# Kernel tuning notes

Hardware: AMD Instinct MI355X
Metric: run time of the kernel (lower is better)

The kernel has to match this reference:

```python
import jax, jax.numpy as jnp
import numpy as np

B, L, H = 4, 2048, 1024
NQ, NKV, D = 8, 2, 256
I, V = 3584, 16384
EPS = 1e-6
THETA = 1e7
ROPE_DIM = 64

def rmsnorm(x, w, eps=EPS):
    xf = x.astype(jnp.float32)
    rms = jax.lax.rsqrt(jnp.mean(xf * xf, axis=-1, keepdims=True) + eps)
    return (xf * rms).astype(x.dtype) * w

def apply_rope(x, positions):
    # x: [B, H, L, D]; rotate first ROPE_DIM dims, interleaved pairs
    n_pairs = ROPE_DIM // 2
    inv_freq = THETA ** (-2.0 * jnp.arange(n_pairs, dtype=jnp.float32) / ROPE_DIM)
    freqs = positions.astype(jnp.float32)[:, None] * inv_freq[None, :]  # [L, n_pairs]
    cos = jnp.cos(freqs)[None, None, :, :]
    sin = jnp.sin(freqs)[None, None, :, :]
    b, h, l, d = x.shape
    xr = x[..., :ROPE_DIM].reshape(b, h, l, n_pairs, 2)
    x0, x1 = xr[..., 0], xr[..., 1]
    r0 = x0 * cos - x1 * sin
    r1 = x0 * sin + x1 * cos
    rotated = jnp.stack([r0, r1], axis=-1).reshape(b, h, l, ROPE_DIM)
    return jnp.concatenate([rotated, x[..., ROPE_DIM:]], axis=-1)

def setup_inputs() -> dict:
    key = jax.random.key(0)
    ks = jax.random.split(key, 12)
    s = 0.02
    return {
        "embeddings": jax.random.normal(ks[0], (B, L, H), jnp.float32),
        "hidden_states": jax.random.normal(ks[1], (B, L, H), jnp.float32),
        "pre_emb_w": jnp.ones((H,), jnp.float32),
        "pre_hid_w": jnp.ones((H,), jnp.float32),
        "fc_w": jax.random.normal(ks[2], (H, 2 * H), jnp.float32) * s,
        "in_ln_w": jnp.ones((H,), jnp.float32),
        "q_w": jax.random.normal(ks[3], (2 * NQ * D, H), jnp.float32) * s,
        "k_w": jax.random.normal(ks[4], (NKV * D, H), jnp.float32) * s,
        "v_w": jax.random.normal(ks[5], (NKV * D, H), jnp.float32) * s,
        "o_w": jax.random.normal(ks[6], (H, NQ * D), jnp.float32) * s,
        "qn_w": jnp.ones((D,), jnp.float32),
        "kn_w": jnp.ones((D,), jnp.float32),
        "post_ln_w": jnp.ones((H,), jnp.float32),
        "gate_w": jax.random.normal(ks[7], (I, H), jnp.float32) * s,
        "up_w": jax.random.normal(ks[8], (I, H), jnp.float32) * s,
        "down_w": jax.random.normal(ks[9], (H, I), jnp.float32) * s,
        "norm_w": jnp.ones((H,), jnp.float32),
        "lm_w": jax.random.normal(ks[10], (V, H), jnp.float32) * s,
    }

def _attention(x, q_w, k_w, v_w, o_w, qn_w, kn_w):
    b, l, _ = x.shape
    qg = (x @ q_w.T).reshape(b, l, NQ, 2, D)
    q = qg[:, :, :, 0, :]
    gate = qg[:, :, :, 1, :]
    k = (x @ k_w.T).reshape(b, l, NKV, D)
    v = (x @ v_w.T).reshape(b, l, NKV, D)
    q = rmsnorm(q, qn_w)
    k = rmsnorm(k, kn_w)
    groups = NQ // NKV
    k = jnp.repeat(k, groups, axis=2)  # [B, L, NQ, D]
    v = jnp.repeat(v, groups, axis=2)
    q, k, v = (t.transpose(0, 2, 1, 3) for t in (q, k, v))  # [B, NQ, L, D]
    positions = jnp.arange(l)
    q = apply_rope(q, positions)
    k = apply_rope(k, positions)
    scores = jnp.einsum('bhqd,bhkd->bhqk', q, k) / jnp.sqrt(jnp.float32(D))
    causal = jnp.tril(jnp.ones((l, l), jnp.bool_))
    scores = jnp.where(causal[None, None], scores, jnp.finfo(scores.dtype).min)
    attn = jax.nn.softmax(scores, axis=-1)
    out = jnp.einsum('bhqk,bhkd->bhqd', attn, v)
    out = out.transpose(0, 2, 1, 3).reshape(b, l, NQ * D)
    out = out * jax.nn.sigmoid(gate.reshape(b, l, NQ * D))
    return out @ o_w.T

def reference(embeddings, hidden_states, pre_emb_w, pre_hid_w, fc_w, in_ln_w,
              q_w, k_w, v_w, o_w, qn_w, kn_w, post_ln_w, gate_w, up_w, down_w,
              norm_w, lm_w):
    x = jnp.concatenate([rmsnorm(embeddings, pre_emb_w),
                         rmsnorm(hidden_states, pre_hid_w)], axis=-1)
    x = x @ fc_w.T
    residual = x
    x = rmsnorm(x, in_ln_w)
    x = _attention(x, q_w, k_w, v_w, o_w, qn_w, kn_w)
    x = residual + x
    residual = x
    x = rmsnorm(x, post_ln_w)
    x = (jax.nn.silu(x @ gate_w.T) * (x @ up_w.T)) @ down_w.T
    x = residual + x
    x = rmsnorm(x, norm_w)
    return x @ lm_w.T
```

## Files before the change

kernel.cpp:

```cpp
#include <hip/hip_runtime.h>

typedef __bf16 bf16;
typedef __bf16 bf16x8 __attribute__((ext_vector_type(8)));
typedef __bf16 bf16x4 __attribute__((ext_vector_type(4)));
typedef float f32x4 __attribute__((ext_vector_type(4)));

__device__ inline f32x4 mfma16(bf16x8 a, bf16x8 b, f32x4 c) {
    return __builtin_amdgcn_mfma_f32_16x16x32_bf16(a, b, c, 0, 0, 0);
}

__device__ __forceinline__ void async_cp16(const void* g, void* l) {
    __builtin_amdgcn_global_load_lds(
        (__attribute__((address_space(1))) char*)g,
        (__attribute__((address_space(3))) char*)l,
        16, 0, 0);
}

__global__ __launch_bounds__(256) void w2b_kernel(const float* __restrict__ s,
                                                  bf16* __restrict__ d)
{
    const size_t i = ((size_t)blockIdx.x * 256 + threadIdx.x) * 4;
    const float4 f = *(const float4*)(s + i);
    bf16x4 t;
    t[0] = (bf16)f.x; t[1] = (bf16)f.y; t[2] = (bf16)f.z; t[3] = (bf16)f.w;
    *(bf16x4*)(d + i) = t;
}

__global__ __launch_bounds__(256) void w2b_qkv_kernel(
    const float* __restrict__ qw, const float* __restrict__ kw,
    const float* __restrict__ vw, bf16* __restrict__ dq)
{
    int bid = blockIdx.x;
    const float* s; bf16* d;
    if (bid < 4096)      { s = qw; d = dq; }
    else if (bid < 4608) { s = kw; d = dq + 4194304; bid -= 4096; }
    else                 { s = vw; d = dq + 4718592; bid -= 4608; }
    const size_t i = ((size_t)bid * 256 + threadIdx.x) * 4;
    const float4 f = *(const float4*)(s + i);
    bf16x4 t;
    t[0] = (bf16)f.x; t[1] = (bf16)f.y; t[2] = (bf16)f.z; t[3] = (bf16)f.w;
    *(bf16x4*)(d + i) = t;
}

__global__ __launch_bounds__(256) void w2b_gu_kernel(
    const float* __restrict__ gw, const float* __restrict__ uw, bf16* __restrict__ dg)
{
    int bid = blockIdx.x;
    const float* s; bf16* d;
    if (bid < 3584) { s = gw; d = dg; }
    else            { s = uw; d = dg + 3670016; bid -= 3584; }
    const size_t i = ((size_t)bid * 256 + threadIdx.x) * 4;
    const float4 f = *(const float4*)(s + i);
    bf16x4 t;
    t[0] = (bf16)f.x; t[1] = (bf16)f.y; t[2] = (bf16)f.z; t[3] = (bf16)f.w;
    *(bf16x4*)(d + i) = t;
}

template <int EPI>
__global__ __launch_bounds__(256) void gemm_kernel(
    const bf16* __restrict__ A, const bf16* __restrict__ B,
    const float* __restrict__ res, float* __restrict__ Cout,
    int M, int N, int K)
{
    __shared__ bf16 As[2][128][64];
    __shared__ bf16 Bs[2][128][64];
    const int tid = threadIdx.x;
    const int wave = tid >> 6, lane = tid & 63;
    const int quad = lane >> 4, l16 = lane & 15;
    const int xsw = l16 & 7;

    const int nby = M >> 7, nbx = N >> 7;
    const int nwg = nbx * nby;
    int bid = blockIdx.x;
    {
        const int q = nwg >> 3, r = nwg & 7;
        const int x = bid & 7, loc = bid >> 3;
        bid = (x < r ? x * (q + 1) : r * (q + 1) + (x - r) * q) + loc;
    }
    const int pg = nbx << 3;
    const int g = bid / pg, rem = bid - g * pg;
    const int by = (g << 3) + (rem & 7);
    const int bx = rem >> 3;
    const int row0 = by << 7, col0 = bx << 7;
    const int wrow = ((wave >> 1) << 6), wcol = ((wave & 1) << 6);

    f32x4 acc[4][4] = {};

    const int srow = tid >> 3;
    const int scol = ((tid & 7) ^ (srow & 7)) * 8;
    const bf16* Ag = A + (size_t)(row0 + srow) * K + scol;
    const bf16* Bg = B + (size_t)(col0 + srow) * K + scol;
    const size_t K32 = (size_t)32 * K;

#define STG128(BUF, KB) do { \
    _Pragma("unroll") for (int q = 0; q < 4; ++q) { \
        async_cp16(Ag + q * K32 + (KB), &As[BUF][0][0] + q * 2048 + wave * 512); \
        async_cp16(Bg + q * K32 + (KB), &Bs[BUF][0][0] + q * 2048 + wave * 512); } } while (0)

    const int NT = K >> 6;
    STG128(0, 0);
    __syncthreads();
    for (int t = 0; t < NT; ++t) {
        const int c = t & 1, n = c ^ 1;
        if (t + 1 < NT) STG128(n, (t + 1) * 64);
        bf16x8 af[8], bfr[8];
#pragma unroll
        for (int i = 0; i < 4; ++i) {
            af[i * 2 + 0] = *(const bf16x8*)(&As[c][wrow + i * 16 + l16][(quad ^ xsw) * 8]);
            af[i * 2 + 1] = *(const bf16x8*)(&As[c][wrow + i * 16 + l16][((4 + quad) ^ xsw) * 8]);
        }
#pragma unroll
        for (int j = 0; j < 4; ++j) {
            bfr[j * 2 + 0] = *(const bf16x8*)(&Bs[c][wcol + j * 16 + l16][(quad ^ xsw) * 8]);
            bfr[j * 2 + 1] = *(const bf16x8*)(&Bs[c][wcol + j * 16 + l16][((4 + quad) ^ xsw) * 8]);
        }
#pragma unroll
        for (int i = 0; i < 4; ++i)
#pragma unroll
            for (int j = 0; j < 4; ++j) {
                acc[i][j] = mfma16(af[i * 2 + 0], bfr[j * 2 + 0], acc[i][j]);
                acc[i][j] = mfma16(af[i * 2 + 1], bfr[j * 2 + 1], acc[i][j]);
            }
        __syncthreads();
    }
#undef STG128

#pragma unroll
    for (int i = 0; i < 4; ++i) {
        const int row = row0 + wrow + i * 16 + quad * 4;
#pragma unroll
        for (int j = 0; j < 4; ++j) {
            const int col = col0 + wcol + j * 16 + l16;
#pragma unroll
            for (int r = 0; r < 4; ++r) {
                const size_t idx = (size_t)(row + r) * N + col;
                float v = acc[i][j][r];
                if (EPI == 1) Cout[idx] = v + res[idx];
                else          Cout[idx] = v;
            }
        }
    }
}

template <int EPI>
__global__ __launch_bounds__(512, 2) void gemm256_kernel(
    const bf16* __restrict__ A, const bf16* __restrict__ B,
    const float* __restrict__ res, float* __restrict__ Cout,
    bf16* __restrict__ hout, int M, int N, int K)
{
    __shared__ bf16 As[2][2][128][64];
    __shared__ bf16 Bs[2][2][128][64];
    const int tid = threadIdx.x;
    const int wid = tid >> 6, lane = tid & 63;
    const int quad = lane >> 4, l16 = lane & 15;
    const int wm = wid >> 2, wn = wid & 3;
    const int xsw = l16 & 7;
    const int bofs = (wn & 1) * 64;

    const int nby = M >> 8, nbx = N >> 8;
    const int nwg = nbx * nby;
    int bid = blockIdx.x;
    {
        const int q = nwg >> 3, r = nwg & 7;
        const int x = bid & 7, loc = bid >> 3;
        bid = (x < r ? x * (q + 1) : r * (q + 1) + (x - r) * q) + loc;
    }
    const int pg = nbx << 3;
    const int g = bid / pg, rem = bid - g * pg;
    const int by = (g << 3) + (rem & 7);
    const int bx = rem >> 3;
    const int row0 = by << 8, col0 = bx << 8;

    const int srow = tid >> 3;
    const int scol = ((tid & 7) ^ ((tid >> 3) & 7)) * 8;
    const bf16* Abase = A + (size_t)(row0 + srow) * K + scol;
    const bf16* Bbase = B + (size_t)(col0 + srow) * K + scol;
    const size_t K64 = (size_t)K * 64;
    const size_t K128 = (size_t)K * 128;

    f32x4 acc[8][4] = {};
    bf16x8 af[8], bf0[4], bf1[4];

#define STG_A(BUF, HH, KB) do { \
    const bf16* _g = Abase + (size_t)(HH) * K128 + (KB); \
    bf16* _l = &As[BUF][HH][0][0] + wid * 512; \
    async_cp16(_g, _l); \
    async_cp16(_g + K64, _l + 4096); } while (0)
#define STG_B(BUF, HH, KB) do { \
    const bf16* _g = Bbase + (size_t)(HH) * K128 + (KB); \
    bf16* _l = &Bs[BUF][HH][0][0] + wid * 512; \
    async_cp16(_g, _l); \
    async_cp16(_g + K64, _l + 4096); } while (0)

#define RD_A(BUF, RH) do { \
    const bf16 (*Ah_)[64] = As[BUF][wm]; \
    _Pragma("unroll") for (int f = 0; f < 4; ++f) { \
        af[f*2+0] = *(const bf16x8*)(&Ah_[(RH)*64 + f*16 + l16][(quad ^ xsw) * 8]); \
        af[f*2+1] = *(const bf16x8*)(&Ah_[(RH)*64 + f*16 + l16][((4 + quad) ^ xsw) * 8]); } } while (0)

#define RD_B(BUF, CH, BF) do { \
    const bf16 (*Bh_)[64] = Bs[BUF][wn >> 1]; \
    _Pragma("unroll") for (int f = 0; f < 2; ++f) { \
        BF[f*2+0] = *(const bf16x8*)(&Bh_[bofs + (CH)*32 + f*16 + l16][(quad ^ xsw) * 8]); \
        BF[f*2+1] = *(const bf16x8*)(&Bh_[bofs + (CH)*32 + f*16 + l16][((4 + quad) ^ xsw) * 8]); } } while (0)

#define MFMA_Q(RH, CH, BF) do { \
    _Pragma("unroll") for (int f = 0; f < 4; ++f) \
    _Pragma("unroll") for (int f2 = 0; f2 < 2; ++f2) { \
        acc[(RH)*4+f][(CH)*2+f2] = mfma16(af[f*2+0], BF[f2*2+0], acc[(RH)*4+f][(CH)*2+f2]); \
        acc[(RH)*4+f][(CH)*2+f2] = mfma16(af[f*2+1], BF[f2*2+1], acc[(RH)*4+f][(CH)*2+f2]); } } while (0)

    const int NT = K >> 6;
    STG_A(0, 0, 0); STG_A(0, 1, 0); STG_B(0, 0, 0); STG_B(0, 1, 0);
    if (NT > 1) {
        STG_A(1, 0, 64); STG_A(1, 1, 64); STG_B(1, 0, 64); STG_B(1, 1, 64);
        asm volatile("s_waitcnt vmcnt(8)" ::: "memory");
    } else {
        asm volatile("s_waitcnt vmcnt(0)" ::: "memory");
    }
    __builtin_amdgcn_sched_barrier(0);
    __builtin_amdgcn_s_barrier();
    RD_A(0, 0); RD_B(0, 0, bf0); RD_B(0, 1, bf1);
    __builtin_amdgcn_sched_barrier(0);

    for (int t = 0; t < NT; ++t) {
        const int c = t & 1, n = c ^ 1;
        const int kb1 = (t + 1) << 6, kb2 = (t + 2) << 6;
        if (t >= 1 && t + 1 < NT) { STG_A(n, 0, kb1); STG_A(n, 1, kb1); }
        asm volatile("s_waitcnt lgkmcnt(4)" ::: "memory");
        __builtin_amdgcn_sched_barrier(0);
        __builtin_amdgcn_s_setprio(1);
        MFMA_Q(0, 0, bf0);
        __builtin_amdgcn_s_setprio(0);
        asm volatile("s_waitcnt lgkmcnt(0)" ::: "memory");
        __builtin_amdgcn_sched_barrier(0);
        __builtin_amdgcn_s_setprio(1);
        MFMA_Q(0, 1, bf1);
        __builtin_amdgcn_s_setprio(0);
        RD_A(c, 1);
        __builtin_amdgcn_sched_barrier(0);
        __builtin_amdgcn_s_barrier();
        if (t + 2 < NT) { STG_B(c, 0, kb2); STG_B(c, 1, kb2); }
        asm volatile("s_waitcnt lgkmcnt(0)" ::: "memory");
        __builtin_amdgcn_sched_barrier(0);
        __builtin_amdgcn_s_setprio(1);
        MFMA_Q(1, 0, bf0);
        MFMA_Q(1, 1, bf1);
        __builtin_amdgcn_s_setprio(0);
        if (t + 1 < NT) {
            if (t + 2 < NT) { asm volatile("s_waitcnt vmcnt(4)" ::: "memory"); }
            else            { asm volatile("s_waitcnt vmcnt(0)" ::: "memory"); }
            __builtin_amdgcn_sched_barrier(0);
            RD_A(n, 0); RD_B(n, 0, bf0); RD_B(n, 1, bf1);
            __builtin_amdgcn_sched_barrier(0);
        }
        __builtin_amdgcn_s_barrier();
    }
#undef STG_A
#undef STG_B
#undef RD_A
#undef RD_B
#undef MFMA_Q

#pragma unroll
    for (int fr = 0; fr < 8; ++fr) {
        const int row = row0 + wm * 128 + fr * 16 + quad * 4;
#pragma unroll
        for (int fc = 0; fc < 4; ++fc) {
            const int col = col0 + wn * 64 + fc * 16 + l16;
#pragma unroll
            for (int r = 0; r < 4; ++r) {
                const size_t idx = (size_t)(row + r) * N + col;
                float v = acc[fr][fc][r];
                if (EPI == 1) {
                    Cout[idx] = v + res[idx];
                } else if (EPI == 2) {
                    const float gg = res[idx];
                    hout[idx] = (bf16)(gg * (1.f / (1.f + __expf(-gg))) * v);
                } else {
                    Cout[idx] = v;
                }
            }
        }
    }
}

__global__ __launch_bounds__(256) void prenorm_kernel(
    const float* __restrict__ emb, const float* __restrict__ hid,
    const float* __restrict__ we, const float* __restrict__ wh,
    bf16* __restrict__ xcat)
{
    const int rr = blockIdx.x * 4 + (threadIdx.x >> 6);
    const int lane = threadIdx.x & 63;
    const int half = rr & 1, row = rr >> 1;
    const float* x = (half ? hid : emb) + (size_t)row * 1024;
    const float* w = half ? wh : we;
    float4 v[4]; float ss = 0.f;
#pragma unroll
    for (int j = 0; j < 4; ++j) {
        v[j] = *(const float4*)(x + (size_t)(lane + 64 * j) * 4);
        ss += v[j].x * v[j].x + v[j].y * v[j].y + v[j].z * v[j].z + v[j].w * v[j].w;
    }
#pragma unroll
    for (int m = 32; m; m >>= 1) ss += __shfl_xor(ss, m, 64);
    const float rms = rsqrtf(ss * (1.f / 1024.f) + 1e-6f);
    bf16* o = xcat + (size_t)row * 2048 + half * 1024;
#pragma unroll
    for (int j = 0; j < 4; ++j) {
        const int d = (lane + 64 * j) * 4;
        float4 wv = *(const float4*)(w + d);
        bf16x4 t;
        t[0] = (bf16)(v[j].x * rms * wv.x);
        t[1] = (bf16)(v[j].y * rms * wv.y);
        t[2] = (bf16)(v[j].z * rms * wv.z);
        t[3] = (bf16)(v[j].w * rms * wv.w);
        *(bf16x4*)(o + d) = t;
    }
}

__global__ __launch_bounds__(256) void rmsnorm_kernel(
    const float* __restrict__ xin, const float* __restrict__ w, bf16* __restrict__ out)
{
    const int row = blockIdx.x * 4 + (threadIdx.x >> 6);
    const int lane = threadIdx.x & 63;
    const float* x = xin + (size_t)row * 1024;
    float4 v[4]; float ss = 0.f;
#pragma unroll
    for (int j = 0; j < 4; ++j) {
        v[j] = *(const float4*)(x + (size_t)(lane + 64 * j) * 4);
        ss += v[j].x * v[j].x + v[j].y * v[j].y + v[j].z * v[j].z + v[j].w * v[j].w;
    }
#pragma unroll
    for (int m = 32; m; m >>= 1) ss += __shfl_xor(ss, m, 64);
    const float rms = rsqrtf(ss * (1.f / 1024.f) + 1e-6f);
    bf16* o = out + (size_t)row * 1024;
#pragma unroll
    for (int j = 0; j < 4; ++j) {
        const int d = (lane + 64 * j) * 4;
        float4 wv = *(const float4*)(w + d);
        bf16x4 t;
        t[0] = (bf16)(v[j].x * rms * wv.x);
        t[1] = (bf16)(v[j].y * rms * wv.y);
        t[2] = (bf16)(v[j].z * rms * wv.z);
        t[3] = (bf16)(v[j].w * rms * wv.w);
        *(bf16x4*)(o + d) = t;
    }
}

__global__ __launch_bounds__(256) void qprep_kernel(
    const float* __restrict__ qg, const float* __restrict__ qn_w, bf16* __restrict__ qa)
{
    const int row = blockIdx.x * 4 + (threadIdx.x >> 6);
    const int lane = threadIdx.x & 63;
    const int h = row & 7, bl = row >> 3;
    const int l = bl & 2047, b = bl >> 11;
    const float* x = qg + (size_t)row * 512;
    float4 v = *(const float4*)(x + lane * 4);
    float ss = v.x * v.x + v.y * v.y + v.z * v.z + v.w * v.w;
#pragma unroll
    for (int m = 32; m; m >>= 1) ss += __shfl_xor(ss, m, 64);
    const float rms = rsqrtf(ss * (1.f / 256.f) + 1e-6f);
    const float4 wv = *(const float4*)(qn_w + lane * 4);
    float y0 = v.x * rms * wv.x, y1 = v.y * rms * wv.y;
    float y2 = v.z * rms * wv.z, y3 = v.w * rms * wv.w;
    if (lane < 16) {
        const float inv0 = powf(1e7f, -(float)(4 * lane) * (1.f / 64.f));
        const float inv1 = powf(1e7f, -(float)(4 * lane + 2) * (1.f / 64.f));
        const float a0 = (float)l * inv0, a1 = (float)l * inv1;
        const float c0 = cosf(a0), s0 = sinf(a0), c1 = cosf(a1), s1 = sinf(a1);
        const float r0 = y0 * c0 - y1 * s0, r1 = y0 * s0 + y1 * c0;
        const float r2 = y2 * c1 - y3 * s1, r3 = y2 * s1 + y3 * c1;
        y0 = r0; y1 = r1; y2 = r2; y3 = r3;
    }
    bf16* o = qa + ((size_t)((b * 8 + h) * 2048 + l)) * 256 + lane * 4;
    bf16x4 t;
    t[0] = (bf16)(y0 * 0.0625f); t[1] = (bf16)(y1 * 0.0625f);
    t[2] = (bf16)(y2 * 0.0625f); t[3] = (bf16)(y3 * 0.0625f);
    *(bf16x4*)o = t;
}

__global__ __launch_bounds__(256) void kprep_kernel(
    const float* __restrict__ kvf, const float* __restrict__ kn_w, bf16* __restrict__ ka)
{
    const int row = blockIdx.x * 4 + (threadIdx.x >> 6);
    const int lane = threadIdx.x & 63;
    const int kv = row & 1, bl = row >> 1;
    const int l = bl & 2047, b = bl >> 11;
    const float* x = kvf + (size_t)bl * 1024 + kv * 256;
    float4 v = *(const float4*)(x + lane * 4);
    float ss = v.x * v.x + v.y * v.y + v.z * v.z + v.w * v.w;
#pragma unroll
    for (int m = 32; m; m >>= 1) ss += __shfl_xor(ss, m, 64);
    const float rms = rsqrtf(ss * (1.f / 256.f) + 1e-6f);
    const float4 wv = *(const float4*)(kn_w + lane * 4);
    float y0 = v.x * rms * wv.x, y1 = v.y * rms * wv.y;
    float y2 = v.z * rms * wv.z, y3 = v.w * rms * wv.w;
    if (lane < 16) {
        const float inv0 = powf(1e7f, -(float)(4 * lane) * (1.f / 64.f));
        const float inv1 = powf(1e7f, -(float)(4 * lane + 2) * (1.f / 64.f));
        const float a0 = (float)l * inv0, a1 = (float)l * inv1;
        const float c0 = cosf(a0), s0 = sinf(a0), c1 = cosf(a1), s1 = sinf(a1);
        const float r0 = y0 * c0 - y1 * s0, r1 = y0 * s0 + y1 * c0;
        const float r2 = y2 * c1 - y3 * s1, r3 = y2 * s1 + y3 * c1;
        y0 = r0; y1 = r1; y2 = r2; y3 = r3;
    }
    bf16* o = ka + ((size_t)((b * 2 + kv) * 2048 + l)) * 256 + lane * 4;
    bf16x4 t;
    t[0] = (bf16)y0; t[1] = (bf16)y1; t[2] = (bf16)y2; t[3] = (bf16)y3;
    *(bf16x4*)o = t;
}

__global__ __launch_bounds__(256) void vprep_kernel(const float* __restrict__ kvf,
                                                    bf16* __restrict__ vt)
{
    __shared__ float t[64][65];
    const int l0 = blockIdx.x << 6;
    const int d0 = blockIdx.y << 6;
    const int b = blockIdx.z >> 1, kv = blockIdx.z & 1;
    const int tx = threadIdx.x & 63, ty = threadIdx.x >> 6;
    const float* src = kvf + (size_t)b * 2048 * 1024 + 512 + kv * 256;
#pragma unroll
    for (int j = 0; j < 16; ++j) {
        const int l = ty + j * 4;
        t[l][tx] = src[(size_t)(l0 + l) * 1024 + d0 + tx];
    }
    __syncthreads();
    bf16* dst = vt + (size_t)(b * 2 + kv) * 256 * 2048;
#pragma unroll
    for (int j = 0; j < 16; ++j) {
        const int d = ty + j * 4;
        dst[(size_t)(d0 + d) * 2048 + l0 + tx] = (bf16)t[tx][d];
    }
}

__global__ __launch_bounds__(256) void attn_kernel(
    const bf16* __restrict__ qa, const bf16* __restrict__ ka,
    const bf16* __restrict__ vt, const float* __restrict__ qg,
    bf16* __restrict__ ag)
{
    __shared__ bf16 Ks[32 * 256];
    __shared__ bf16 Vt[256 * 32];
    __shared__ bf16 Pw[4 * 16 * 32];
    const int tid = threadIdx.x;
    const int wave = tid >> 6, lane = tid & 63;
    const int quad = lane >> 4, l16 = lane & 15;
    const int bid = blockIdx.x;
    const int j = bid & 15, h = (bid >> 4) & 7, b = bid >> 7;
    const int kvh = h >> 2;
    const bf16* qptr = qa + ((size_t)(b * 8 + h)) * 2048 * 256;
    const bf16* kptr = ka + ((size_t)(b * 2 + kvh)) * 2048 * 256;
    const bf16* vptr = vt + ((size_t)(b * 2 + kvh)) * 256 * 2048;

    for (int s = 0; s < 2; ++s) {
        const int qt = s ? (31 - j) : j;
        const int qbase = qt * 64 + wave * 16;

        bf16x8 qf[8];
#pragma unroll
        for (int db = 0; db < 8; ++db)
            qf[db] = *(const bf16x8*)(qptr + (size_t)(qbase + l16) * 256 + db * 32 + quad * 8);

        f32x4 o_acc[16] = {};
        float m_i[4], l_i[4];
#pragma unroll
        for (int r = 0; r < 4; ++r) { m_i[r] = -1e30f; l_i[r] = 0.f; }

        const int ntiles = qt * 2 + 2;
        for (int kt = 0; kt < ntiles; ++kt) {
            const int kvs = kt * 32;
#pragma unroll
            for (int c = 0; c < 4; ++c) {
                const int idx = tid + c * 256;
                const int kr = idx >> 5, kc32 = idx & 31;
                *(bf16x8*)(&Ks[kr * 256 + (kc32 ^ (kr & 7)) * 8]) =
                    *(const bf16x8*)(kptr + (size_t)(kvs + kr) * 256 + kc32 * 8);
                const int vd = idx >> 2, vc = (idx & 3) * 8;
                *(bf16x8*)(&Vt[vd * 32 + vc]) = *(const bf16x8*)(vptr + (size_t)vd * 2048 + kvs + vc);
            }
            __syncthreads();

            f32x4 s0 = {}, s1 = {};
#pragma unroll
            for (int db = 0; db < 8; ++db) {
                const int ch = (db * 4 + quad) ^ (l16 & 7);
                bf16x8 k0 = *(const bf16x8*)(&Ks[l16 * 256 + ch * 8]);
                bf16x8 k1 = *(const bf16x8*)(&Ks[(16 + l16) * 256 + ch * 8]);
                s0 = mfma16(qf[db], k0, s0);
                s1 = mfma16(qf[db], k1, s1);
            }

            float alpha[4], p0v[4], p1v[4];
#pragma unroll
            for (int r = 0; r < 4; ++r) {
                const int qrow = qbase + quad * 4 + r;
                float a0 = (kvs + l16 > qrow) ? -1e30f : s0[r];
                float a1 = (kvs + 16 + l16 > qrow) ? -1e30f : s1[r];
                float mx = fmaxf(a0, a1);
#pragma unroll
                for (int m = 8; m; m >>= 1) mx = fmaxf(mx, __shfl_xor(mx, m, 64));
                const float mnew = fmaxf(m_i[r], mx);
                const float a = __expf(m_i[r] - mnew);
                const float p0 = __expf(a0 - mnew);
                const float p1 = __expf(a1 - mnew);
                float ps = p0 + p1;
#pragma unroll
                for (int m = 8; m; m >>= 1) ps += __shfl_xor(ps, m, 64);
                l_i[r] = l_i[r] * a + ps;
                m_i[r] = mnew;
                alpha[r] = a; p0v[r] = p0; p1v[r] = p1;
            }
#pragma unroll
            for (int t = 0; t < 16; ++t) {
                f32x4 o = o_acc[t];
                o[0] *= alpha[0]; o[1] *= alpha[1]; o[2] *= alpha[2]; o[3] *= alpha[3];
                o_acc[t] = o;
            }
            bf16* pw = &Pw[wave * 16 * 32];
#pragma unroll
            for (int r = 0; r < 4; ++r) {
                pw[(quad * 4 + r) * 32 + l16]      = (bf16)p0v[r];
                pw[(quad * 4 + r) * 32 + 16 + l16] = (bf16)p1v[r];
            }
            __syncthreads();
            const bf16x8 pa = *(const bf16x8*)(&pw[l16 * 32 + quad * 8]);
#pragma unroll
            for (int t = 0; t < 16; ++t) {
                bf16x8 vfr = *(const bf16x8*)(&Vt[(t * 16 + l16) * 32 + quad * 8]);
                o_acc[t] = mfma16(pa, vfr, o_acc[t]);
            }
            __syncthreads();
        }

#pragma unroll
        for (int r = 0; r < 4; ++r) {
            const float inv = 1.f / l_i[r];
            const int row = qbase + quad * 4 + r;
            const float* gr = qg + ((size_t)((b * 2048 + row) * 8 + h)) * 512 + 256;
            bf16* ar = ag + ((size_t)(b * 2048 + row)) * 2048 + h * 256;
#pragma unroll
            for (int t = 0; t < 16; ++t) {
                const int d = t * 16 + l16;
                const float o = o_acc[t][r] * inv;
                const float gg = gr[d];
                ar[d] = (bf16)(o * (1.f / (1.f + __expf(-gg))));
            }
        }
    }
}

extern "C" void kernel_launch(void* const* d_in, const int* in_sizes, int n_in,
                              void* d_out, int out_size, void* d_ws, size_t ws_size,
                              hipStream_t stream)
{
    const float* emb       = (const float*)d_in[0];
    const float* hid       = (const float*)d_in[1];
    const float* pre_emb_w = (const float*)d_in[2];
    const float* pre_hid_w = (const float*)d_in[3];
    const float* fc_w      = (const float*)d_in[4];
    const float* in_ln_w   = (const float*)d_in[5];
    const float* q_w       = (const float*)d_in[6];
    const float* k_w       = (const float*)d_in[7];
    const float* v_w       = (const float*)d_in[8];
    const float* o_w       = (const float*)d_in[9];
    const float* qn_w      = (const float*)d_in[10];
    const float* kn_w      = (const float*)d_in[11];
    const float* post_ln_w = (const float*)d_in[12];
    const float* gate_w    = (const float*)d_in[13];
    const float* up_w      = (const float*)d_in[14];
    const float* down_w    = (const float*)d_in[15];
    const float* norm_w    = (const float*)d_in[16];
    const float* lm_w      = (const float*)d_in[17];
    float* out = (float*)d_out;
    char* ws = (char*)d_ws;

    float* xres = (float*)(ws + 0);
    bf16*  xln  = (bf16*)(ws + 33554432);
    char*  C    = ws + 50331648;
    char*  D    = ws + 184549376;
    char*  E    = ws + 318767104;
    float* qg   = (float*)C;
    float* gf   = (float*)C;
    bf16*  xcat = (bf16*)D;
    float* kvf  = (float*)(D + 33554432);
    bf16*  ag   = (bf16*)(D + 67108864);
    bf16*  qa   = (bf16*)E;
    bf16*  ka   = (bf16*)(E + 33554432);
    bf16*  va   = (bf16*)(E + 41943040);
    bf16*  hb   = (bf16*)E;
    bf16*  wbC  = (bf16*)C;
    bf16*  wbD  = (bf16*)D;
    bf16*  wkv  = (bf16*)D + 4194304;
    bf16*  wbDt = (bf16*)(D + 117440512);

    prenorm_kernel<<<4096, 256, 0, stream>>>(emb, hid, pre_emb_w, pre_hid_w, xcat);

    w2b_kernel<<<2048, 256, 0, stream>>>(fc_w, wbC);
    gemm_kernel<0><<<512, 256, 0, stream>>>(xcat, wbC, nullptr, xres, 8192, 1024, 2048);
    rmsnorm_kernel<<<2048, 256, 0, stream>>>(xres, in_ln_w, xln);

    w2b_qkv_kernel<<<5120, 256, 0, stream>>>(q_w, k_w, v_w, wbD);
    gemm256_kernel<0><<<512, 512, 0, stream>>>(xln, wbD, nullptr, qg, nullptr, 8192, 4096, 1024);
    gemm_kernel<0><<<512, 256, 0, stream>>>(xln, wkv, nullptr, kvf, 8192, 1024, 1024);

    qprep_kernel<<<16384, 256, 0, stream>>>(qg, qn_w, qa);
    kprep_kernel<<<4096, 256, 0, stream>>>(kvf, kn_w, ka);
    vprep_kernel<<<dim3(32, 4, 8), 256, 0, stream>>>(kvf, va);
    attn_kernel<<<512, 256, 0, stream>>>(qa, ka, va, qg, ag);

    w2b_kernel<<<2048, 256, 0, stream>>>(o_w, wbC);
    gemm_kernel<1><<<512, 256, 0, stream>>>(ag, wbC, xres, xres, 8192, 1024, 2048);
    rmsnorm_kernel<<<2048, 256, 0, stream>>>(xres, post_ln_w, xln);

    w2b_gu_kernel<<<7168, 256, 0, stream>>>(gate_w, up_w, wbDt);
    gemm256_kernel<0><<<448, 512, 0, stream>>>(xln, wbDt, nullptr, gf, nullptr, 8192, 3584, 1024);
    gemm256_kernel<2><<<448, 512, 0, stream>>>(xln, wbDt + 3670016, gf, nullptr, hb, 8192, 3584, 1024);

    w2b_kernel<<<3584, 256, 0, stream>>>(down_w, wbC);
    gemm_kernel<1><<<512, 256, 0, stream>>>(hb, wbC, xres, xres, 8192, 1024, 3584);
    rmsnorm_kernel<<<2048, 256, 0, stream>>>(xres, norm_w, xln);

    w2b_kernel<<<16384, 256, 0, stream>>>(lm_w, wbC);
    gemm256_kernel<0><<<2048, 512, 0, stream>>>(xln, wbC, nullptr, out, nullptr, 8192, 16384, 1024);
}
```

Measured before the change: 1.710 ms.

## Merge elementwise launches and add lazy softmax rescaling in attention

Several small launches are combined into multi-role kernels: prenorm with the fc weight cast, each rmsnorm with the following weight cast, the q/k/v prep kernels into one, and the down and lm weight casts into one. The attention kernel now rescales the running max only when a new max exceeds the old by more than 8, which skips most accumulator rescales. It also replaces a block-wide barrier with a wave-local LDS wait, and adds an occupancy hint to launch bounds. The aim is to cut launch and tail overhead and to trim softmax ALU and sync cost. The risks are extra workspace aliasing for the lm weights and the reliance on per-wave LDS ordering.

```diff
diff --git a/kernel.cpp b/kernel.cpp
--- a/kernel.cpp
+++ b/kernel.cpp
@@ -16,25 +16,10 @@
         16, 0, 0);
 }
 
-__global__ __launch_bounds__(256) void w2b_kernel(const float* __restrict__ s,
-                                                  bf16* __restrict__ d)
-{
-    const size_t i = ((size_t)blockIdx.x * 256 + threadIdx.x) * 4;
-    const float4 f = *(const float4*)(s + i);
-    bf16x4 t;
-    t[0] = (bf16)f.x; t[1] = (bf16)f.y; t[2] = (bf16)f.z; t[3] = (bf16)f.w;
-    *(bf16x4*)(d + i) = t;
-}
-
-__global__ __launch_bounds__(256) void w2b_qkv_kernel(
-    const float* __restrict__ qw, const float* __restrict__ kw,
-    const float* __restrict__ vw, bf16* __restrict__ dq)
-{
-    int bid = blockIdx.x;
-    const float* s; bf16* d;
-    if (bid < 4096)      { s = qw; d = dq; }
-    else if (bid < 4608) { s = kw; d = dq + 4194304; bid -= 4096; }
-    else                 { s = vw; d = dq + 4718592; bid -= 4608; }
+
+__device__ __forceinline__ void w2b_blk(const float* __restrict__ s,
+                                        bf16* __restrict__ d, int bid)
+{
     const size_t i = ((size_t)bid * 256 + threadIdx.x) * 4;
     const float4 f = *(const float4*)(s + i);
     bf16x4 t;
@@ -42,18 +27,200 @@
     *(bf16x4*)(d + i) = t;
 }
 
-__global__ __launch_bounds__(256) void w2b_gu_kernel(
+__device__ __forceinline__ void rmsnorm_blk(const float* __restrict__ xin,
+                                            const float* __restrict__ w,
+                                            bf16* __restrict__ out, int bid)
+{
+    const int row = bid * 4 + (threadIdx.x >> 6);
+    const int lane = threadIdx.x & 63;
+    const float* x = xin + (size_t)row * 1024;
+    float4 v[4]; float ss = 0.f;
+#pragma unroll
+    for (int j = 0; j < 4; ++j) {
+        v[j] = *(const float4*)(x + (size_t)(lane + 64 * j) * 4);
+        ss += v[j].x * v[j].x + v[j].y * v[j].y + v[j].z * v[j].z + v[j].w * v[j].w;
+    }
+#pragma unroll
+    for (int m = 32; m; m >>= 1) ss += __shfl_xor(ss, m, 64);
+    const float rms = rsqrtf(ss * (1.f / 1024.f) + 1e-6f);
+    bf16* o = out + (size_t)row * 1024;
+#pragma unroll
+    for (int j = 0; j < 4; ++j) {
+        const int d = (lane + 64 * j) * 4;
+        float4 wv = *(const float4*)(w + d);
+        bf16x4 t;
+        t[0] = (bf16)(v[j].x * rms * wv.x);
+        t[1] = (bf16)(v[j].y * rms * wv.y);
+        t[2] = (bf16)(v[j].z * rms * wv.z);
+        t[3] = (bf16)(v[j].w * rms * wv.w);
+        *(bf16x4*)(o + d) = t;
+    }
+}
+
+
+__global__ __launch_bounds__(256) void prenorm_fc_kernel(
+    const float* __restrict__ emb, const float* __restrict__ hid,
+    const float* __restrict__ we, const float* __restrict__ wh,
+    bf16* __restrict__ xcat, const float* __restrict__ fcw, bf16* __restrict__ wfc)
+{
+    if (blockIdx.x >= 4096) { w2b_blk(fcw, wfc, blockIdx.x - 4096); return; }
+    const int rr = blockIdx.x * 4 + (threadIdx.x >> 6);
+    const int lane = threadIdx.x & 63;
+    const int half = rr & 1, row = rr >> 1;
+    const float* x = (half ? hid : emb) + (size_t)row * 1024;
+    const float* w = half ? wh : we;
+    float4 v[4]; float ss = 0.f;
+#pragma unroll
+    for (int j = 0; j < 4; ++j) {
+        v[j] = *(const float4*)(x + (size_t)(lane + 64 * j) * 4);
+        ss += v[j].x * v[j].x + v[j].y * v[j].y + v[j].z * v[j].z + v[j].w * v[j].w;
+    }
+#pragma unroll
+    for (int m = 32; m; m >>= 1) ss += __shfl_xor(ss, m, 64);
+    const float rms = rsqrtf(ss * (1.f / 1024.f) + 1e-6f);
+    bf16* o = xcat + (size_t)row * 2048 + half * 1024;
+#pragma unroll
+    for (int j = 0; j < 4; ++j) {
+        const int d = (lane + 64 * j) * 4;
+        float4 wv = *(const float4*)(w + d);
+        bf16x4 t;
+        t[0] = (bf16)(v[j].x * rms * wv.x);
+        t[1] = (bf16)(v[j].y * rms * wv.y);
+        t[2] = (bf16)(v[j].z * rms * wv.z);
+        t[3] = (bf16)(v[j].w * rms * wv.w);
+        *(bf16x4*)(o + d) = t;
+    }
+}
+
+__global__ __launch_bounds__(256) void norm_qkv_kernel(
+    const float* __restrict__ xres, const float* __restrict__ lnw, bf16* __restrict__ xln,
+    const float* __restrict__ qw, const float* __restrict__ kw,
+    const float* __restrict__ vw, bf16* __restrict__ dq)
+{
+    int bid = blockIdx.x;
+    if (bid < 2048) { rmsnorm_blk(xres, lnw, xln, bid); return; }
+    bid -= 2048;
+    if (bid < 4096)      w2b_blk(qw, dq, bid);
+    else if (bid < 4608) w2b_blk(kw, dq + 4194304, bid - 4096);
+    else                 w2b_blk(vw, dq + 4718592, bid - 4608);
+}
+
+__global__ __launch_bounds__(256) void norm_gu_kernel(
+    const float* __restrict__ xres, const float* __restrict__ lnw, bf16* __restrict__ xln,
     const float* __restrict__ gw, const float* __restrict__ uw, bf16* __restrict__ dg)
 {
     int bid = blockIdx.x;
-    const float* s; bf16* d;
-    if (bid < 3584) { s = gw; d = dg; }
-    else            { s = uw; d = dg + 3670016; bid -= 3584; }
-    const size_t i = ((size_t)bid * 256 + threadIdx.x) * 4;
-    const float4 f = *(const float4*)(s + i);
-    bf16x4 t;
-    t[0] = (bf16)f.x; t[1] = (bf16)f.y; t[2] = (bf16)f.z; t[3] = (bf16)f.w;
-    *(bf16x4*)(d + i) = t;
+    if (bid < 2048) { rmsnorm_blk(xres, lnw, xln, bid); return; }
+    bid -= 2048;
+    if (bid < 3584) w2b_blk(gw, dg, bid);
+    else            w2b_blk(uw, dg + 3670016, bid - 3584);
+}
+
+__global__ __launch_bounds__(256) void w2b_downlm_kernel(
+    const float* __restrict__ dw, bf16* __restrict__ ddown,
+    const float* __restrict__ lw, bf16* __restrict__ dlm)
+{
+    int bid = blockIdx.x;
+    if (bid < 3584) w2b_blk(dw, ddown, bid);
+    else            w2b_blk(lw, dlm, bid - 3584);
+}
+
+__global__ __launch_bounds__(256) void rmsnorm_kernel(
+    const float* __restrict__ xin, const float* __restrict__ w, bf16* __restrict__ out)
+{
+    rmsnorm_blk(xin, w, out, blockIdx.x);
+}
+
+__global__ __launch_bounds__(256) void w2b_kernel(const float* __restrict__ s,
+                                                  bf16* __restrict__ d)
+{
+    w2b_blk(s, d, blockIdx.x);
+}
+
+__global__ __launch_bounds__(256) void prep_kernel(
+    const float* __restrict__ qg, const float* __restrict__ qn_w, bf16* __restrict__ qa,
+    const float* __restrict__ kvf, const float* __restrict__ kn_w,
+    bf16* __restrict__ ka, bf16* __restrict__ va)
+{
+    __shared__ float tsh[64][65];
+    const int gbid = blockIdx.x;
+    if (gbid < 16384) {
+        const int row = gbid * 4 + (threadIdx.x >> 6);
+        const int lane = threadIdx.x & 63;
+        const int h = row & 7, bl = row >> 3;
+        const int l = bl & 2047, b = bl >> 11;
+        const float* x = qg + (size_t)row * 512;
+        float4 v = *(const float4*)(x + lane * 4);
+        float ss = v.x * v.x + v.y * v.y + v.z * v.z + v.w * v.w;
+#pragma unroll
+        for (int m = 32; m; m >>= 1) ss += __shfl_xor(ss, m, 64);
+        const float rms = rsqrtf(ss * (1.f / 256.f) + 1e-6f);
+        const float4 wv = *(const float4*)(qn_w + lane * 4);
+        float y0 = v.x * rms * wv.x, y1 = v.y * rms * wv.y;
+        float y2 = v.z * rms * wv.z, y3 = v.w * rms * wv.w;
+        if (lane < 16) {
+            const float inv0 = powf(1e7f, -(float)(4 * lane) * (1.f / 64.f));
+            const float inv1 = powf(1e7f, -(float)(4 * lane + 2) * (1.f / 64.f));
+            const float a0 = (float)l * inv0, a1 = (float)l * inv1;
+            const float c0 = cosf(a0), s0 = sinf(a0), c1 = cosf(a1), s1 = sinf(a1);
+            const float r0 = y0 * c0 - y1 * s0, r1 = y0 * s0 + y1 * c0;
+            const float r2 = y2 * c1 - y3 * s1, r3 = y2 * s1 + y3 * c1;
+            y0 = r0; y1 = r1; y2 = r2; y3 = r3;
+        }
+        bf16* o = qa + ((size_t)((b * 8 + h) * 2048 + l)) * 256 + lane * 4;
+        bf16x4 t;
+        t[0] = (bf16)(y0 * 0.0625f); t[1] = (bf16)(y1 * 0.0625f);
+        t[2] = (bf16)(y2 * 0.0625f); t[3] = (bf16)(y3 * 0.0625f);
+        *(bf16x4*)o = t;
+    } else if (gbid < 20480) {
+        const int bid = gbid - 16384;
+        const int row = bid * 4 + (threadIdx.x >> 6);
+        const int lane = threadIdx.x & 63;
+        const int kv = row & 1, bl = row >> 1;
+        const int l = bl & 2047, b = bl >> 11;
+        const float* x = kvf + (size_t)bl * 1024 + kv * 256;
+        float4 v = *(const float4*)(x + lane * 4);
+        float ss = v.x * v.x + v.y * v.y + v.z * v.z + v.w * v.w;
+#pragma unroll
+        for (int m = 32; m; m >>= 1) ss += __shfl_xor(ss, m, 64);
+        const float rms = rsqrtf(ss * (1.f / 256.f) + 1e-6f);
+        const float4 wv = *(const float4*)(kn_w + lane * 4);
+        float y0 = v.x * rms * wv.x, y1 = v.y * rms * wv.y;
+        float y2 = v.z * rms * wv.z, y3 = v.w * rms * wv.w;
+        if (lane < 16) {
+            const float inv0 = powf(1e7f, -(float)(4 * lane) * (1.f / 64.f));
+            const float inv1 = powf(1e7f, -(float)(4 * lane + 2) * (1.f / 64.f));
+            const float a0 = (float)l * inv0, a1 = (float)l * inv1;
+            const float c0 = cosf(a0), s0 = sinf(a0), c1 = cosf(a1), s1 = sinf(a1);
+            const float r0 = y0 * c0 - y1 * s0, r1 = y0 * s0 + y1 * c0;
+            const float r2 = y2 * c1 - y3 * s1, r3 = y2 * s1 + y3 * c1;
+            y0 = r0; y1 = r1; y2 = r2; y3 = r3;
+        }
+        bf16* o = ka + ((size_t)((b * 2 + kv) * 2048 + l)) * 256 + lane * 4;
+        bf16x4 t;
+        t[0] = (bf16)y0; t[1] = (bf16)y1; t[2] = (bf16)y2; t[3] = (bf16)y3;
+        *(bf16x4*)o = t;
+    } else {
+        const int vid = gbid - 20480;
+        const int l0 = (vid & 31) << 6;
+        const int d0 = ((vid >> 5) & 3) << 6;
+        const int z = vid >> 7;
+        const int b = z >> 1, kv = z & 1;
+        const int tx = threadIdx.x & 63, ty = threadIdx.x >> 6;
+        const float* src = kvf + (size_t)b * 2048 * 1024 + 512 + kv * 256;
+#pragma unroll
+        for (int j = 0; j < 16; ++j) {
+            const int l = ty + j * 4;
+            tsh[l][tx] = src[(size_t)(l0 + l) * 1024 + d0 + tx];
+        }
+        __syncthreads();
+        bf16* dst = va + (size_t)(b * 2 + kv) * 256 * 2048;
+#pragma unroll
+        for (int j = 0; j < 16; ++j) {
+            const int d = ty + j * 4;
+            dst[(size_t)(d0 + d) * 2048 + l0 + tx] = (bf16)tsh[tx][d];
+        }
+    }
 }
 
 template <int EPI>
@@ -285,155 +452,7 @@
     }
 }
 
-__global__ __launch_bounds__(256) void prenorm_kernel(
-    const float* __restrict__ emb, const float* __restrict__ hid,
-    const float* __restrict__ we, const float* __restrict__ wh,
-    bf16* __restrict__ xcat)
-{
-    const int rr = blockIdx.x * 4 + (threadIdx.x >> 6);
-    const int lane = threadIdx.x & 63;
-    const int half = rr & 1, row = rr >> 1;
-    const float* x = (half ? hid : emb) + (size_t)row * 1024;
-    const float* w = half ? wh : we;
-    float4 v[4]; float ss = 0.f;
-#pragma unroll
-    for (int j = 0; j < 4; ++j) {
-        v[j] = *(const float4*)(x + (size_t)(lane + 64 * j) * 4);
-        ss += v[j].x * v[j].x + v[j].y * v[j].y + v[j].z * v[j].z + v[j].w * v[j].w;
-    }
-#pragma unroll
-    for (int m = 32; m; m >>= 1) ss += __shfl_xor(ss, m, 64);
-    const float rms = rsqrtf(ss * (1.f / 1024.f) + 1e-6f);
-    bf16* o = xcat + (size_t)row * 2048 + half * 1024;
-#pragma unroll
-    for (int j = 0; j < 4; ++j) {
-        const int d = (lane + 64 * j) * 4;
-        float4 wv = *(const float4*)(w + d);
-        bf16x4 t;
-        t[0] = (bf16)(v[j].x * rms * wv.x);
-        t[1] = (bf16)(v[j].y * rms * wv.y);
-        t[2] = (bf16)(v[j].z * rms * wv.z);
-        t[3] = (bf16)(v[j].w * rms * wv.w);
-        *(bf16x4*)(o + d) = t;
-    }
-}
-
-__global__ __launch_bounds__(256) void rmsnorm_kernel(
-    const float* __restrict__ xin, const float* __restrict__ w, bf16* __restrict__ out)
-{
-    const int row = blockIdx.x * 4 + (threadIdx.x >> 6);
-    const int lane = threadIdx.x & 63;
-    const float* x = xin + (size_t)row * 1024;
-    float4 v[4]; float ss = 0.f;
-#pragma unroll
-    for (int j = 0; j < 4; ++j) {
-        v[j] = *(const float4*)(x + (size_t)(lane + 64 * j) * 4);
-        ss += v[j].x * v[j].x + v[j].y * v[j].y + v[j].z * v[j].z + v[j].w * v[j].w;
-    }
-#pragma unroll
-    for (int m = 32; m; m >>= 1) ss += __shfl_xor(ss, m, 64);
-    const float rms = rsqrtf(ss * (1.f / 1024.f) + 1e-6f);
-    bf16* o = out + (size_t)row * 1024;
-#pragma unroll
-    for (int j = 0; j < 4; ++j) {
-        const int d = (lane + 64 * j) * 4;
-        float4 wv = *(const float4*)(w + d);
-        bf16x4 t;
-        t[0] = (bf16)(v[j].x * rms * wv.x);
-        t[1] = (bf16)(v[j].y * rms * wv.y);
-        t[2] = (bf16)(v[j].z * rms * wv.z);
-        t[3] = (bf16)(v[j].w * rms * wv.w);
-        *(bf16x4*)(o + d) = t;
-    }
-}
-
-__global__ __launch_bounds__(256) void qprep_kernel(
-    const float* __restrict__ qg, const float* __restrict__ qn_w, bf16* __restrict__ qa)
-{
-    const int row = blockIdx.x * 4 + (threadIdx.x >> 6);
-    const int lane = threadIdx.x & 63;
-    const int h = row & 7, bl = row >> 3;
-    const int l = bl & 2047, b = bl >> 11;
-    const float* x = qg + (size_t)row * 512;
-    float4 v = *(const float4*)(x + lane * 4);
-    float ss = v.x * v.x + v.y * v.y + v.z * v.z + v.w * v.w;
-#pragma unroll
-    for (int m = 32; m; m >>= 1) ss += __shfl_xor(ss, m, 64);
-    const float rms = rsqrtf(ss * (1.f / 256.f) + 1e-6f);
-    const float4 wv = *(const float4*)(qn_w + lane * 4);
-    float y0 = v.x * rms * wv.x, y1 = v.y * rms * wv.y;
-    float y2 = v.z * rms * wv.z, y3 = v.w * rms * wv.w;
-    if (lane < 16) {
-        const float inv0 = powf(1e7f, -(float)(4 * lane) * (1.f / 64.f));
-        const float inv1 = powf(1e7f, -(float)(4 * lane + 2) * (1.f / 64.f));
-        const float a0 = (float)l * inv0, a1 = (float)l * inv1;
-        const float c0 = cosf(a0), s0 = sinf(a0), c1 = cosf(a1), s1 = sinf(a1);
-        const float r0 = y0 * c0 - y1 * s0, r1 = y0 * s0 + y1 * c0;
-        const float r2 = y2 * c1 - y3 * s1, r3 = y2 * s1 + y3 * c1;
-        y0 = r0; y1 = r1; y2 = r2; y3 = r3;
-    }
-    bf16* o = qa + ((size_t)((b * 8 + h) * 2048 + l)) * 256 + lane * 4;
-    bf16x4 t;
-    t[0] = (bf16)(y0 * 0.0625f); t[1] = (bf16)(y1 * 0.0625f);
-    t[2] = (bf16)(y2 * 0.0625f); t[3] = (bf16)(y3 * 0.0625f);
-    *(bf16x4*)o = t;
-}
-
-__global__ __launch_bounds__(256) void kprep_kernel(
-    const float* __restrict__ kvf, const float* __restrict__ kn_w, bf16* __restrict__ ka)
-{
-    const int row = blockIdx.x * 4 + (threadIdx.x >> 6);
-    const int lane = threadIdx.x & 63;
-    const int kv = row & 1, bl = row >> 1;
-    const int l = bl & 2047, b = bl >> 11;
-    const float* x = kvf + (size_t)bl * 1024 + kv * 256;
-    float4 v = *(const float4*)(x + lane * 4);
-    float ss = v.x * v.x + v.y * v.y + v.z * v.z + v.w * v.w;
-#pragma unroll
-    for (int m = 32; m; m >>= 1) ss += __shfl_xor(ss, m, 64);
-    const float rms = rsqrtf(ss * (1.f / 256.f) + 1e-6f);
-    const float4 wv = *(const float4*)(kn_w + lane * 4);
-    float y0 = v.x * rms * wv.x, y1 = v.y * rms * wv.y;
-    float y2 = v.z * rms * wv.z, y3 = v.w * rms * wv.w;
-    if (lane < 16) {
-        const float inv0 = powf(1e7f, -(float)(4 * lane) * (1.f / 64.f));
-        const float inv1 = powf(1e7f, -(float)(4 * lane + 2) * (1.f / 64.f));
-        const float a0 = (float)l * inv0, a1 = (float)l * inv1;
-        const float c0 = cosf(a0), s0 = sinf(a0), c1 = cosf(a1), s1 = sinf(a1);
-        const float r0 = y0 * c0 - y1 * s0, r1 = y0 * s0 + y1 * c0;
-        const float r2 = y2 * c1 - y3 * s1, r3 = y2 * s1 + y3 * c1;
-        y0 = r0; y1 = r1; y2 = r2; y3 = r3;
-    }
-    bf16* o = ka + ((size_t)((b * 2 + kv) * 2048 + l)) * 256 + lane * 4;
-    bf16x4 t;
-    t[0] = (bf16)y0; t[1] = (bf16)y1; t[2] = (bf16)y2; t[3] = (bf16)y3;
-    *(bf16x4*)o = t;
-}
-
-__global__ __launch_bounds__(256) void vprep_kernel(const float* __restrict__ kvf,
-                                                    bf16* __restrict__ vt)
-{
-    __shared__ float t[64][65];
-    const int l0 = blockIdx.x << 6;
-    const int d0 = blockIdx.y << 6;
-    const int b = blockIdx.z >> 1, kv = blockIdx.z & 1;
-    const int tx = threadIdx.x & 63, ty = threadIdx.x >> 6;
-    const float* src = kvf + (size_t)b * 2048 * 1024 + 512 + kv * 256;
-#pragma unroll
-    for (int j = 0; j < 16; ++j) {
-        const int l = ty + j * 4;
-        t[l][tx] = src[(size_t)(l0 + l) * 1024 + d0 + tx];
-    }
-    __syncthreads();
-    bf16* dst = vt + (size_t)(b * 2 + kv) * 256 * 2048;
-#pragma unroll
-    for (int j = 0; j < 16; ++j) {
-        const int d = ty + j * 4;
-        dst[(size_t)(d0 + d) * 2048 + l0 + tx] = (bf16)t[tx][d];
-    }
-}
-
-__global__ __launch_bounds__(256) void attn_kernel(
+__global__ __launch_bounds__(256, 4) void attn_kernel(
     const bf16* __restrict__ qa, const bf16* __restrict__ ka,
     const bf16* __restrict__ vt, const float* __restrict__ qg,
     bf16* __restrict__ ag)
@@ -489,39 +508,49 @@
                 s1 = mfma16(qf[db], k1, s1);
             }
 
-            float alpha[4], p0v[4], p1v[4];
+            float a0[4], a1[4], mx[4];
 #pragma unroll
             for (int r = 0; r < 4; ++r) {
                 const int qrow = qbase + quad * 4 + r;
-                float a0 = (kvs + l16 > qrow) ? -1e30f : s0[r];
-                float a1 = (kvs + 16 + l16 > qrow) ? -1e30f : s1[r];
-                float mx = fmaxf(a0, a1);
-#pragma unroll
-                for (int m = 8; m; m >>= 1) mx = fmaxf(mx, __shfl_xor(mx, m, 64));
-                const float mnew = fmaxf(m_i[r], mx);
-                const float a = __expf(m_i[r] - mnew);
-                const float p0 = __expf(a0 - mnew);
-                const float p1 = __expf(a1 - mnew);
+                a0[r] = (kvs + l16 > qrow) ? -1e30f : s0[r];
+                a1[r] = (kvs + 16 + l16 > qrow) ? -1e30f : s1[r];
+                float m = fmaxf(a0[r], a1[r]);
+#pragma unroll
+                for (int mm = 8; mm; mm >>= 1) m = fmaxf(m, __shfl_xor(m, mm, 64));
+                mx[r] = m;
+            }
+            const bool big = (mx[0] > m_i[0] + 8.f) | (mx[1] > m_i[1] + 8.f) |
+                             (mx[2] > m_i[2] + 8.f) | (mx[3] > m_i[3] + 8.f);
+            if (__any(big)) {
+                float alpha[4];
+#pragma unroll
+                for (int r = 0; r < 4; ++r) {
+                    const float mnew = fmaxf(m_i[r], mx[r]);
+                    alpha[r] = __expf(m_i[r] - mnew);
+                    m_i[r] = mnew;
+                    l_i[r] *= alpha[r];
+                }
+#pragma unroll
+                for (int t = 0; t < 16; ++t) {
+                    f32x4 o = o_acc[t];
+                    o[0] *= alpha[0]; o[1] *= alpha[1]; o[2] *= alpha[2]; o[3] *= alpha[3];
+                    o_acc[t] = o;
+                }
+            }
+            bf16* pw = &Pw[wave * 16 * 32];
+#pragma unroll
+            for (int r = 0; r < 4; ++r) {
+                const float p0 = __expf(a0[r] - m_i[r]);
+                const float p1 = __expf(a1[r] - m_i[r]);
                 float ps = p0 + p1;
 #pragma unroll
-                for (int m = 8; m; m >>= 1) ps += __shfl_xor(ps, m, 64);
-                l_i[r] = l_i[r] * a + ps;
-                m_i[r] = mnew;
-                alpha[r] = a; p0v[r] = p0; p1v[r] = p1;
-            }
-#pragma unroll
-            for (int t = 0; t < 16; ++t) {
-                f32x4 o = o_acc[t];
-                o[0] *= alpha[0]; o[1] *= alpha[1]; o[2] *= alpha[2]; o[3] *= alpha[3];
-                o_acc[t] = o;
-            }
-            bf16* pw = &Pw[wave * 16 * 32];
-#pragma unroll
-            for (int r = 0; r < 4; ++r) {
-                pw[(quad * 4 + r) * 32 + l16]      = (bf16)p0v[r];
-                pw[(quad * 4 + r) * 32 + 16 + l16] = (bf16)p1v[r];
-            }
-            __syncthreads();
+                for (int mm = 8; mm; mm >>= 1) ps += __shfl_xor(ps, mm, 64);
+                l_i[r] += ps;
+                pw[(quad * 4 + r) * 32 + l16]      = (bf16)p0;
+                pw[(quad * 4 + r) * 32 + 16 + l16] = (bf16)p1;
+            }
+            asm volatile("s_waitcnt lgkmcnt(0)" ::: "memory");
+            __builtin_amdgcn_sched_barrier(0);
             const bf16x8 pa = *(const bf16x8*)(&pw[l16 * 32 + quad * 8]);
 #pragma unroll
             for (int t = 0; t < 16; ++t) {
@@ -588,37 +617,31 @@
     bf16*  va   = (bf16*)(E + 41943040);
     bf16*  hb   = (bf16*)E;
     bf16*  wbC  = (bf16*)C;
+    bf16*  wlm  = (bf16*)(C + 8388608);
     bf16*  wbD  = (bf16*)D;
     bf16*  wkv  = (bf16*)D + 4194304;
     bf16*  wbDt = (bf16*)(D + 117440512);
 
-    prenorm_kernel<<<4096, 256, 0, stream>>>(emb, hid, pre_emb_w, pre_hid_w, xcat);
-
-    w2b_kernel<<<2048, 256, 0, stream>>>(fc_w, wbC);
+    prenorm_fc_kernel<<<6144, 256, 0, stream>>>(emb, hid, pre_emb_w, pre_hid_w,
+                                                xcat, fc_w, wbC);
     gemm_kernel<0><<<512, 256, 0, stream>>>(xcat, wbC, nullptr, xres, 8192, 1024, 2048);
-    rmsnorm_kernel<<<2048, 256, 0, stream>>>(xres, in_ln_w, xln);
-
-    w2b_qkv_kernel<<<5120, 256, 0, stream>>>(q_w, k_w, v_w, wbD);
+
+    norm_qkv_kernel<<<7168, 256, 0, stream>>>(xres, in_ln_w, xln, q_w, k_w, v_w, wbD);
     gemm256_kernel<0><<<512, 512, 0, stream>>>(xln, wbD, nullptr, qg, nullptr, 8192, 4096, 1024);
     gemm_kernel<0><<<512, 256, 0, stream>>>(xln, wkv, nullptr, kvf, 8192, 1024, 1024);
 
-    qprep_kernel<<<16384, 256, 0, stream>>>(qg, qn_w, qa);
-    kprep_kernel<<<4096, 256, 0, stream>>>(kvf, kn_w, ka);
-    vprep_kernel<<<dim3(32, 4, 8), 256, 0, stream>>>(kvf, va);
+    prep_kernel<<<21504, 256, 0, stream>>>(qg, qn_w, qa, kvf, kn_w, ka, va);
     attn_kernel<<<512, 256, 0, stream>>>(qa, ka, va, qg, ag);
 
     w2b_kernel<<<2048, 256, 0, stream>>>(o_w, wbC);
     gemm_kernel<1><<<512, 256, 0, stream>>>(ag, wbC, xres, xres, 8192, 1024, 2048);
-    rmsnorm_kernel<<<2048, 256, 0, stream>>>(xres, post_ln_w, xln);
-
-    w2b_gu_kernel<<<7168, 256, 0, stream>>>(gate_w, up_w, wbDt);
+
+    norm_gu_kernel<<<9216, 256, 0, stream>>>(xres, post_ln_w, xln, gate_w, up_w, wbDt);
     gemm256_kernel<0><<<448, 512, 0, stream>>>(xln, wbDt, nullptr, gf, nullptr, 8192, 3584, 1024);
     gemm256_kernel<2><<<448, 512, 0, stream>>>(xln, wbDt + 3670016, gf, nullptr, hb, 8192, 3584, 1024);
 
-    w2b_kernel<<<3584, 256, 0, stream>>>(down_w, wbC);
+    w2b_downlm_kernel<<<19968, 256, 0, stream>>>(down_w, wbC, lm_w, wlm);
     gemm_kernel<1><<<512, 256, 0, stream>>>(hb, wbC, xres, xres, 8192, 1024, 3584);
     rmsnorm_kernel<<<2048, 256, 0, stream>>>(xres, norm_w, xln);
-
-    w2b_kernel<<<16384, 256, 0, stream>>>(lm_w, wbC);
-    gemm256_kernel<0><<<2048, 512, 0, stream>>>(xln, wbC, nullptr, out, nullptr, 8192, 16384, 1024);
-}
+    gemm256_kernel<0><<<2048, 512, 0, stream>>>(xln, wlm, nullptr, out, nullptr, 8192, 16384, 1024);
+}
```

After: 2.130 ms. +24.6%, slower.
